# Kernel tuning notes

Hardware: AMD Instinct MI355X
Metric: run time of the kernel (lower is better)

Reference implementation:

```python
import jax, jax.numpy as jnp
import numpy as np

D_MODEL, D_K, D_V, H = 1024, 64, 64, 16
LN_EPS = 1e-5


def setup_inputs() -> dict:
    key = jax.random.key(0)
    ks = jax.random.split(key, 16)
    B, NQ, NK = 2, 1024, 1024
    queries = jax.random.normal(ks[0], (B, NQ, D_MODEL), dtype=jnp.float32)
    keys = jax.random.normal(ks[1], (B, NK, D_MODEL), dtype=jnp.float32)
    values = jax.random.normal(ks[2], (B, NK, D_MODEL), dtype=jnp.float32)
    attention_mask = jax.random.randint(ks[3], (B, H, NQ, NK), 0, 2).astype(jnp.bool_)
    attention_weights = jax.random.uniform(ks[4], (B, H, NQ, NK), dtype=jnp.float32)
    # Linear params, stored (in, out) so x @ W + b
    def xavier(k, shape):
        lim = float(np.sqrt(6.0 / (shape[0] + shape[1])))
        return jax.random.uniform(k, shape, jnp.float32, -lim, lim)
    Wq = xavier(ks[5], (D_MODEL, H * D_K)); bq = jnp.zeros((H * D_K,), jnp.float32)
    Wk = xavier(ks[6], (D_MODEL, H * D_K)); bk = jnp.zeros((H * D_K,), jnp.float32)
    Wv = xavier(ks[7], (D_MODEL, H * D_V)); bv = jnp.zeros((H * D_V,), jnp.float32)
    Wo = xavier(ks[8], (H * D_V, D_MODEL)); bo = jnp.zeros((D_MODEL,), jnp.float32)
    gamma = jnp.ones((D_MODEL,), jnp.float32)
    beta = jnp.zeros((D_MODEL,), jnp.float32)
    return dict(queries=queries, keys=keys, values=values,
                attention_mask=attention_mask, attention_weights=attention_weights,
                Wq=Wq, bq=bq, Wk=Wk, bk=bk, Wv=Wv, bv=bv, Wo=Wo, bo=bo,
                gamma=gamma, beta=beta)


def layer_norm(x, gamma, beta):
    mu = jnp.mean(x, axis=-1, keepdims=True)
    var = jnp.mean(jnp.square(x - mu), axis=-1, keepdims=True)
    return (x - mu) * jax.lax.rsqrt(var + LN_EPS) * gamma + beta


def reference(queries, keys, values, attention_mask, attention_weights,
              Wq, bq, Wk, bk, Wv, bv, Wo, bo, gamma, beta):
    B, NQ, _ = queries.shape
    NK = keys.shape[1]
    q = (queries @ Wq + bq).reshape(B, NQ, H, D_K).transpose(0, 2, 1, 3)  # b h nq dk
    k = (keys @ Wk + bk).reshape(B, NK, H, D_K).transpose(0, 2, 1, 3)    # b h nk dk
    v = (values @ Wv + bv).reshape(B, NK, H, D_V).transpose(0, 2, 1, 3)  # b h nk dv
    att = jnp.einsum('bhqd,bhkd->bhqk', q, k) / jnp.sqrt(jnp.float32(D_K))
    att = att * attention_weights
    att = jnp.where(attention_mask, -jnp.inf, att)
    att = jax.nn.softmax(att, axis=-1)  # dropout is identity in eval
    out = jnp.einsum('bhqk,bhkd->bhqd', att, v)
    out = out.transpose(0, 2, 1, 3).reshape(B, NQ, H * D_V)
    out = out @ Wo + bo
    # post-LN residual (identity_map_reordering=False)
    return layer_norm(queries + out, gamma, beta)
```

## Files before the change

kernel.cpp:

```cpp
#include <hip/hip_runtime.h>
#include <hip/hip_bf16.h>
#include <math.h>

#define B_   2
#define H_   16
#define NSEQ 1024
#define DM   1024
#define DKV  64
#define NSPLIT 4
#define KPB  (NSEQ / NSPLIT)
#define LNEPS 1e-5f

typedef __attribute__((ext_vector_type(8))) short s16x8;
typedef __attribute__((ext_vector_type(4))) float f32x4;
typedef __attribute__((ext_vector_type(4))) unsigned u32x4;

__device__ inline short f2bf(float f) {
    __hip_bfloat16 h = __float2bfloat16(f);
    return *reinterpret_cast<short*>(&h);
}
__device__ inline float bf2f(short s) {
    unsigned u = ((unsigned)(unsigned short)s) << 16;
    return __uint_as_float(u);
}

__device__ __forceinline__ void gll16(const void* g, void* l) {
    __builtin_amdgcn_global_load_lds(
        (const __attribute__((address_space(1))) unsigned int*)g,
        (__attribute__((address_space(3))) unsigned int*)l, 16, 0, 0);
}

#define SYNC_STAGE do { asm volatile("s_waitcnt vmcnt(0)" ::: "memory"); __syncthreads(); } while (0)

__global__ void detect_mask(const unsigned* __restrict__ mask_words, int* __restrict__ flag) {
    unsigned f = 0;
    for (int i = 0; i < 256; ++i) f |= (mask_words[i] > 1u) ? 1u : 0u;
    *flag = (int)f;
}

__global__ __launch_bounds__(256) void castT4_bf16(
    const float* __restrict__ w0, const float* __restrict__ w1,
    const float* __restrict__ w2, const float* __restrict__ w3,
    short* __restrict__ t0, short* __restrict__ t1,
    short* __restrict__ t2, short* __restrict__ t3) {
    const float* W = blockIdx.z == 0 ? w0 : (blockIdx.z == 1 ? w1 : (blockIdx.z == 2 ? w2 : w3));
    short* Wt      = blockIdx.z == 0 ? t0 : (blockIdx.z == 1 ? t1 : (blockIdx.z == 2 ? t2 : t3));
    __shared__ float tl[32][33];
    const int k0 = blockIdx.y * 32, n0 = blockIdx.x * 32;
    const int r = threadIdx.x >> 3, c4 = (threadIdx.x & 7) * 4;
    *(float4*)&tl[r][c4] = *(const float4*)(W + (size_t)(k0 + r) * DM + n0 + c4);
    __syncthreads();
    unsigned u0 = (unsigned short)f2bf(tl[c4+0][r]) | ((unsigned)(unsigned short)f2bf(tl[c4+1][r]) << 16);
    unsigned u1 = (unsigned short)f2bf(tl[c4+2][r]) | ((unsigned)(unsigned short)f2bf(tl[c4+3][r]) << 16);
    uint2 pk; pk.x = u0; pk.y = u1;
    *(uint2*)(Wt + (size_t)(n0 + r) * DM + k0 + c4) = pk;
}

__device__ inline void loadAf32(const float* p, s16x8& a0, s16x8& a1) {
    f32x4 v0 = *(const f32x4*)p,       v1 = *(const f32x4*)(p + 4);
    f32x4 v2 = *(const f32x4*)(p + 8), v3 = *(const f32x4*)(p + 12);
    a0[0]=f2bf(v0[0]); a0[1]=f2bf(v0[1]); a0[2]=f2bf(v0[2]); a0[3]=f2bf(v0[3]);
    a0[4]=f2bf(v1[0]); a0[5]=f2bf(v1[1]); a0[6]=f2bf(v1[2]); a0[7]=f2bf(v1[3]);
    a1[0]=f2bf(v2[0]); a1[1]=f2bf(v2[1]); a1[2]=f2bf(v2[2]); a1[3]=f2bf(v2[3]);
    a1[4]=f2bf(v3[0]); a1[5]=f2bf(v3[1]); a1[6]=f2bf(v3[2]); a1[7]=f2bf(v3[3]);
}

__global__ __launch_bounds__(256) void gemm_qkv(
    const float* __restrict__ qin, const float* __restrict__ kin, const float* __restrict__ vin,
    const short* __restrict__ Wcat,
    const float* __restrict__ bq, const float* __restrict__ bk, const float* __restrict__ bv,
    short* __restrict__ Qh, short* __restrict__ Kh, short* __restrict__ Vth)
{
    const int t  = threadIdx.x;
    const int wv = t >> 6, l = t & 63, lg = l >> 4, li = l & 15;
    const int wr = wv >> 1, wc = wv & 1;
    const int c0g = blockIdx.x * 64, m0 = blockIdx.y * 64;
    const int sel = c0g >> 10;
    const int c0  = c0g & 1023;
    const float* A    = sel == 0 ? qin : (sel == 1 ? kin : vin);
    const short* Wt   = Wcat + (size_t)sel * DM * DM;
    const float* bias = sel == 0 ? bq : (sel == 1 ? bk : bv);
    short* outp       = sel == 0 ? Qh : (sel == 1 ? Kh : Vth);
    const int mode    = sel == 2 ? 2 : 1;

    __shared__ short Asl[64 * 64];
    __shared__ short Bsl[64 * 64];

    f32x4 acc[2][2] = {};
    const int sr = t >> 2, scol = (t & 3) * 16;
    const int sw = (sr & 7) << 3;

    s16x8 a0, a1;
    loadAf32(A + (size_t)(m0 + sr) * DM + scol, a0, a1);
    s16x8 b0 = *(const s16x8*)(Wt + (size_t)(c0 + sr) * DM + scol);
    s16x8 b1 = *(const s16x8*)(Wt + (size_t)(c0 + sr) * DM + scol + 8);

    for (int k0 = 0; k0 < DM; k0 += 64) {
        __syncthreads();
        *(s16x8*)&Asl[sr * 64 + (scol ^ sw)]       = a0;
        *(s16x8*)&Asl[sr * 64 + ((scol + 8) ^ sw)] = a1;
        *(s16x8*)&Bsl[sr * 64 + (scol ^ sw)]       = b0;
        *(s16x8*)&Bsl[sr * 64 + ((scol + 8) ^ sw)] = b1;
        __syncthreads();
        if (k0 + 64 < DM) {
            loadAf32(A + (size_t)(m0 + sr) * DM + k0 + 64 + scol, a0, a1);
            b0 = *(const s16x8*)(Wt + (size_t)(c0 + sr) * DM + k0 + 64 + scol);
            b1 = *(const s16x8*)(Wt + (size_t)(c0 + sr) * DM + k0 + 64 + scol + 8);
        }
        #pragma unroll
        for (int kh = 0; kh < 2; ++kh) {
            s16x8 af[2], bf[2];
            #pragma unroll
            for (int fi = 0; fi < 2; ++fi) {
                const int row = wr * 32 + fi * 16 + li;
                af[fi] = *(const s16x8*)&Asl[row * 64 + ((kh * 32 + lg * 8) ^ ((row & 7) << 3))];
            }
            #pragma unroll
            for (int fj = 0; fj < 2; ++fj) {
                const int row = wc * 32 + fj * 16 + li;
                bf[fj] = *(const s16x8*)&Bsl[row * 64 + ((kh * 32 + lg * 8) ^ ((row & 7) << 3))];
            }
            #pragma unroll
            for (int fi = 0; fi < 2; ++fi)
                #pragma unroll
                for (int fj = 0; fj < 2; ++fj)
                    acc[fi][fj] = __builtin_amdgcn_mfma_f32_16x16x32_bf16(af[fi], bf[fj], acc[fi][fj], 0, 0, 0);
        }
    }

    const int hh = c0 >> 6;
    #pragma unroll
    for (int fi = 0; fi < 2; ++fi) {
        #pragma unroll
        for (int j = 0; j < 4; ++j) {
            const int m = m0 + wr * 32 + fi * 16 + lg * 4 + j;
            const int bb = m >> 10, n = m & (NSEQ - 1);
            #pragma unroll
            for (int fj = 0; fj < 2; ++fj) {
                const int cc = wc * 32 + fj * 16 + li;
                float v = acc[fi][fj][j] + bias[c0 + cc];
                if (mode == 1)
                    outp[(((size_t)(bb * H_ + hh) * NSEQ) + n) * DKV + cc] = f2bf(v);
                else
                    outp[(((size_t)(bb * H_ + hh) * DKV) + cc) * NSEQ + n] = f2bf(v);
            }
        }
    }
}

__global__ __launch_bounds__(256) void gemm_out(
    const short* __restrict__ A, const short* __restrict__ Wt,
    const float* __restrict__ bias, const float* __restrict__ resid,
    float* __restrict__ outp)
{
    const int t  = threadIdx.x;
    const int wv = t >> 6, l = t & 63, lg = l >> 4, li = l & 15;
    const int wr = wv >> 1, wc = wv & 1;
    const int c0 = blockIdx.x * 64, m0 = blockIdx.y * 64;

    __shared__ short Asl[64 * 64];
    __shared__ short Bsl[64 * 64];

    f32x4 acc[2][2] = {};
    const int sr = t >> 2, scol = (t & 3) * 16;
    const int sw = (sr & 7) << 3;

    s16x8 a0 = *(const s16x8*)(A + (size_t)(m0 + sr) * DM + scol);
    s16x8 a1 = *(const s16x8*)(A + (size_t)(m0 + sr) * DM + scol + 8);
    s16x8 b0 = *(const s16x8*)(Wt + (size_t)(c0 + sr) * DM + scol);
    s16x8 b1 = *(const s16x8*)(Wt + (size_t)(c0 + sr) * DM + scol + 8);

    for (int k0 = 0; k0 < DM; k0 += 64) {
        __syncthreads();
        *(s16x8*)&Asl[sr * 64 + (scol ^ sw)]       = a0;
        *(s16x8*)&Asl[sr * 64 + ((scol + 8) ^ sw)] = a1;
        *(s16x8*)&Bsl[sr * 64 + (scol ^ sw)]       = b0;
        *(s16x8*)&Bsl[sr * 64 + ((scol + 8) ^ sw)] = b1;
        __syncthreads();
        if (k0 + 64 < DM) {
            a0 = *(const s16x8*)(A + (size_t)(m0 + sr) * DM + k0 + 64 + scol);
            a1 = *(const s16x8*)(A + (size_t)(m0 + sr) * DM + k0 + 64 + scol + 8);
            b0 = *(const s16x8*)(Wt + (size_t)(c0 + sr) * DM + k0 + 64 + scol);
            b1 = *(const s16x8*)(Wt + (size_t)(c0 + sr) * DM + k0 + 64 + scol + 8);
        }
        #pragma unroll
        for (int kh = 0; kh < 2; ++kh) {
            s16x8 af[2], bf[2];
            #pragma unroll
            for (int fi = 0; fi < 2; ++fi) {
                const int row = wr * 32 + fi * 16 + li;
                af[fi] = *(const s16x8*)&Asl[row * 64 + ((kh * 32 + lg * 8) ^ ((row & 7) << 3))];
            }
            #pragma unroll
            for (int fj = 0; fj < 2; ++fj) {
                const int row = wc * 32 + fj * 16 + li;
                bf[fj] = *(const s16x8*)&Bsl[row * 64 + ((kh * 32 + lg * 8) ^ ((row & 7) << 3))];
            }
            #pragma unroll
            for (int fi = 0; fi < 2; ++fi)
                #pragma unroll
                for (int fj = 0; fj < 2; ++fj)
                    acc[fi][fj] = __builtin_amdgcn_mfma_f32_16x16x32_bf16(af[fi], bf[fj], acc[fi][fj], 0, 0, 0);
        }
    }

    #pragma unroll
    for (int fi = 0; fi < 2; ++fi) {
        #pragma unroll
        for (int j = 0; j < 4; ++j) {
            const int m = m0 + wr * 32 + fi * 16 + lg * 4 + j;
            #pragma unroll
            for (int fj = 0; fj < 2; ++fj) {
                const int c = c0 + wc * 32 + fj * 16 + li;
                outp[(size_t)m * DM + c] = acc[fi][fj][j] + bias[c] + resid[(size_t)m * DM + c];
            }
        }
    }
}

__global__ __launch_bounds__(256) void attn_split(
    const short* __restrict__ Qb, const short* __restrict__ Kb, const short* __restrict__ Vt,
    const void* __restrict__ mask, const float* __restrict__ wgt,
    const int* __restrict__ flagp, short* __restrict__ Opart,
    float* __restrict__ mpart, float* __restrict__ lpart)
{
    const int t  = threadIdx.x;
    const int wv = t >> 6;
    const int l  = t & 63;
    const int lg = l >> 4;
    const int li = l & 15;
    const int qt = blockIdx.x >> 2;
    const int sp = blockIdx.x & (NSPLIT-1);
    const int h  = blockIdx.y, b = blockIdx.z;
    const size_t bh = (size_t)b * H_ + h;
    const int qrow = qt*64 + wv*16 + li;
    const int kbase = sp * KPB;

    __shared__ short Kl[8 * 512];
    __shared__ short Vl[8 * 512];
    __shared__ float Wl[16 * 256];
    __shared__ unsigned char Ml[4 * 1024];
    __shared__ short Plds[4][16][80];

    const short* Qp = Qb + (bh * NSEQ + qt*64 + wv*16) * DKV;
    const short* Kp = Kb + bh * NSEQ * DKV;
    const short* Vp = Vt + bh * DKV * NSEQ;
    const size_t moff = (bh * NSEQ + qrow) * NSEQ;
    const size_t rowT = bh * NSEQ + (size_t)qt * 64;
    const int mmode = *flagp;
    const unsigned* Mi = (const unsigned*)mask;
    const unsigned char* Mb = (const unsigned char*)mask;

    const int srow = l >> 4;
    const int schk = (l & 15) ^ srow;
    const int mrow = l >> 2;
    const int mchk = l & 3;

    s16x8 qa[2];
    qa[0] = *(const s16x8*)(Qp + (size_t)li * DKV + lg*8);
    qa[1] = *(const s16x8*)(Qp + (size_t)li * DKV + 32 + lg*8);

    float m_run = -1e30f, l_run = 0.f;
    f32x4 oacc[4] = {};
    const int rq = li >> 2, rs = li & 3;

    for (int c = 0; c < NSPLIT; ++c) {
        const int kc = kbase + c * 64;

        __syncthreads();
        if (wv == 0) {
            #pragma unroll
            for (int i = 0; i < 8; ++i) {
                const int nt = i & 3, dc = i >> 2;
                gll16(Kp + (size_t)(kc + nt*16 + li) * DKV + dc*32 + lg*8, Kl + i*512);
            }
        } else if (wv == 1) {
            #pragma unroll
            for (int i = 0; i < 8; ++i) {
                const int dt = i & 3, kch = i >> 2;
                gll16(Vp + (size_t)(dt*16 + li) * NSEQ + kc + kch*32 + lg*8, Vl + i*512);
            }
        } else if (wv == 2) {
            #pragma unroll
            for (int j = 0; j < 8; ++j)
                gll16(wgt + (rowT + j*4 + srow) * NSEQ + kc + schk*4, Wl + j*256);
            #pragma unroll
            for (int j = 0; j < 2; ++j)
                gll16(Mb + (rowT + j*16 + mrow) * NSEQ + kc + mchk*16, Ml + j*1024);
        } else {
            #pragma unroll
            for (int j = 8; j < 16; ++j)
                gll16(wgt + (rowT + j*4 + srow) * NSEQ + kc + schk*4, Wl + j*256);
            #pragma unroll
            for (int j = 2; j < 4; ++j)
                gll16(Mb + (rowT + j*16 + mrow) * NSEQ + kc + mchk*16, Ml + j*1024);
        }
        SYNC_STAGE;

        f32x4 sc[4] = {};
        #pragma unroll
        for (int dc = 0; dc < 2; ++dc)
            #pragma unroll
            for (int nt = 0; nt < 4; ++nt) {
                s16x8 kb = *(const s16x8*)&Kl[(dc*4 + nt)*512 + l*8];
                sc[nt] = __builtin_amdgcn_mfma_f32_16x16x32_bf16(kb, qa[dc], sc[nt], 0, 0, 0);
            }

        float sv[16];
        float cmax = -1e30f;
        #pragma unroll
        for (int nt = 0; nt < 4; ++nt) {
            const int pos = ((nt*4 + lg) ^ rs) * 4;
            f32x4 w4 = *(const f32x4*)&Wl[(wv*4 + rq)*256 + rs*64 + pos];
            unsigned mm[4];
            if (mmode) {
                unsigned u = *(const unsigned*)&Ml[wv*1024 + (li*4 + nt)*16 + lg*4];
                mm[0] = u & 0xffu; mm[1] = (u >> 8) & 0xffu;
                mm[2] = (u >> 16) & 0xffu; mm[3] = u >> 24;
            } else {
                u32x4 mi = *(const u32x4*)(Mi + moff + kc + nt*16 + lg*4);
                mm[0] = mi[0]; mm[1] = mi[1]; mm[2] = mi[2]; mm[3] = mi[3];
            }
            #pragma unroll
            for (int r = 0; r < 4; ++r) {
                float s = sc[nt][r] * 0.125f * w4[r];
                s = mm[r] ? -1e30f : s;
                sv[nt*4 + r] = s;
                cmax = fmaxf(cmax, s);
            }
        }
        cmax = fmaxf(cmax, __shfl_xor(cmax, 16));
        cmax = fmaxf(cmax, __shfl_xor(cmax, 32));
        const float mnew = fmaxf(m_run, cmax);
        const float factor = __expf(m_run - mnew);
        m_run = mnew;

        float csum = 0.f;
        #pragma unroll
        for (int nt = 0; nt < 4; ++nt) {
            float p0 = __expf(sv[nt*4+0] - mnew), p1 = __expf(sv[nt*4+1] - mnew);
            float p2 = __expf(sv[nt*4+2] - mnew), p3 = __expf(sv[nt*4+3] - mnew);
            csum += p0 + p1 + p2 + p3;
            unsigned u0 = (unsigned short)f2bf(p0) | ((unsigned)(unsigned short)f2bf(p1) << 16);
            unsigned u1 = (unsigned short)f2bf(p2) | ((unsigned)(unsigned short)f2bf(p3) << 16);
            uint2 pk; pk.x = u0; pk.y = u1;
            *(uint2*)&Plds[wv][li][nt*16 + lg*4] = pk;
        }
        csum += __shfl_xor(csum, 16);
        csum += __shfl_xor(csum, 32);
        l_run = l_run * factor + csum;

        float ffac[4];
        #pragma unroll
        for (int r = 0; r < 4; ++r) ffac[r] = __shfl(factor, lg*4 + r);
        #pragma unroll
        for (int dt = 0; dt < 4; ++dt)
            #pragma unroll
            for (int r = 0; r < 4; ++r)
                oacc[dt][r] *= ffac[r];

        #pragma unroll
        for (int kch = 0; kch < 2; ++kch) {
            s16x8 pa = *(const s16x8*)&Plds[wv][li][kch*32 + lg*8];
            #pragma unroll
            for (int dt = 0; dt < 4; ++dt) {
                s16x8 vb = *(const s16x8*)&Vl[(kch*4 + dt)*512 + l*8];
                oacc[dt] = __builtin_amdgcn_mfma_f32_16x16x32_bf16(pa, vb, oacc[dt], 0, 0, 0);
            }
        }
    }

    const size_t SBH = (size_t)B_ * H_ * NSEQ;
    if (lg == 0) {
        mpart[(size_t)sp * SBH + bh * NSEQ + qrow] = m_run;
        lpart[(size_t)sp * SBH + bh * NSEQ + qrow] = l_run;
    }
    #pragma unroll
    for (int dt = 0; dt < 4; ++dt)
        #pragma unroll
        for (int r = 0; r < 4; ++r)
            Opart[((size_t)sp * SBH + bh * NSEQ + qt*64 + wv*16 + lg*4 + r) * DKV + dt*16 + li]
                = f2bf(oacc[dt][r]);
}

__global__ __launch_bounds__(256, 1) void attn_combine(
    const short* __restrict__ Opart, const float* __restrict__ mpart,
    const float* __restrict__ lpart, short* __restrict__ Ob)
{
    const size_t SBH = (size_t)B_ * H_ * NSEQ;
    const int R = blockIdx.x * 4 + (threadIdx.x >> 6);
    const int d = threadIdx.x & 63;
    const int bh = R >> 10, n = R & (NSEQ - 1);
    const int b = bh >> 4, h = bh & (H_ - 1);

    float ms[NSPLIT], ls[NSPLIT], ov[NSPLIT];
    #pragma unroll
    for (int s = 0; s < NSPLIT; ++s) {
        ms[s] = mpart[(size_t)s * SBH + R];
        ls[s] = lpart[(size_t)s * SBH + R];
        ov[s] = bf2f(Opart[((size_t)s * SBH + R) * DKV + d]);
    }
    float mstar = -1e30f;
    #pragma unroll
    for (int s = 0; s < NSPLIT; ++s) mstar = fmaxf(mstar, ms[s]);
    float lstar = 0.f, acc = 0.f;
    #pragma unroll
    for (int s = 0; s < NSPLIT; ++s) {
        float w = __expf(ms[s] - mstar);
        lstar += w * ls[s];
        acc   += w * ov[s];
    }
    Ob[((size_t)b * NSEQ + n) * DM + h * DKV + d] = f2bf(acc / lstar);
}

__global__ __launch_bounds__(256) void ln_kernel(
    const float* __restrict__ Y, const float* __restrict__ gamma,
    const float* __restrict__ beta, float* __restrict__ out)
{
    const int row = blockIdx.x;
    const int t = threadIdx.x;
    const float* y = Y + (size_t)row * DM;
    float4 x = *(const float4*)(y + t*4);
    __shared__ float red[4];
    float s = x.x + x.y + x.z + x.w;
    #pragma unroll
    for (int off = 32; off > 0; off >>= 1) s += __shfl_xor(s, off);
    if ((t & 63) == 0) red[t >> 6] = s;
    __syncthreads();
    float mean = (red[0]+red[1]+red[2]+red[3]) * (1.0f/DM);
    float d0 = x.x-mean, d1 = x.y-mean, d2 = x.z-mean, d3 = x.w-mean;
    float sq = d0*d0 + d1*d1 + d2*d2 + d3*d3;
    __syncthreads();
    #pragma unroll
    for (int off = 32; off > 0; off >>= 1) sq += __shfl_xor(sq, off);
    if ((t & 63) == 0) red[t >> 6] = sq;
    __syncthreads();
    float var = (red[0]+red[1]+red[2]+red[3]) * (1.0f/DM);
    float rstd = rsqrtf(var + LNEPS);
    int c = t * 4;
    float4 g  = *(const float4*)(gamma + c);
    float4 bb = *(const float4*)(beta + c);
    float4 o;
    o.x = d0*rstd*g.x + bb.x;
    o.y = d1*rstd*g.y + bb.y;
    o.z = d2*rstd*g.z + bb.z;
    o.w = d3*rstd*g.w + bb.w;
    *(float4*)(out + (size_t)row*DM + c) = o;
}

extern "C" void kernel_launch(void* const* d_in, const int* in_sizes, int n_in,
                              void* d_out, int out_size, void* d_ws, size_t ws_size,
                              hipStream_t stream)
{
    const float* queries = (const float*)d_in[0];
    const float* keys    = (const float*)d_in[1];
    const float* values  = (const float*)d_in[2];
    const void*  mask    = d_in[3];
    const float* wgt     = (const float*)d_in[4];
    const float* Wq = (const float*)d_in[5];  const float* bq = (const float*)d_in[6];
    const float* Wk = (const float*)d_in[7];  const float* bk = (const float*)d_in[8];
    const float* Wv = (const float*)d_in[9];  const float* bv = (const float*)d_in[10];
    const float* Wo = (const float*)d_in[11]; const float* bo = (const float*)d_in[12];
    const float* gamma = (const float*)d_in[13]; const float* beta = (const float*)d_in[14];
    float* out = (float*)d_out;

    const size_t SZ  = (size_t)B_ * NSEQ * DM;
    const size_t WSZ = (size_t)DM * DM;
    const size_t SBH = (size_t)B_ * H_ * NSEQ;

    char* ws = (char*)d_ws;
    int*   flag = (int*)ws;
    short* Wtq = (short*)(ws + 256);
    short* Wtk = Wtq + WSZ;
    short* Wtv = Wtk + WSZ;
    short* Wto = Wtv + WSZ;
    short* Qh  = Wto + WSZ;
    short* Kh  = Qh + SZ;
    short* Vth = Kh + SZ;
    short* Opart = Vth + SZ;
    float* mpart = (float*)(Opart + (size_t)NSPLIT * SBH * DKV);
    float* lpart = mpart + NSPLIT * SBH;
    short* Ob  = (short*)(lpart + NSPLIT * SBH);
    float* Yb  = (float*)Opart;

    detect_mask<<<1, 1, 0, stream>>>((const unsigned*)mask, flag);
    castT4_bf16<<<dim3(32, 32, 4), 256, 0, stream>>>(Wq, Wk, Wv, Wo, Wtq, Wtk, Wtv, Wto);

    gemm_qkv<<<dim3(48, 32), 256, 0, stream>>>(queries, keys, values, Wtq,
                                               bq, bk, bv, Qh, Kh, Vth);

    attn_split<<<dim3(16 * NSPLIT, H_, B_), 256, 0, stream>>>(
        Qh, Kh, Vth, mask, wgt, flag, Opart, mpart, lpart);
    attn_combine<<<dim3((int)(SBH / 4)), 256, 0, stream>>>(Opart, mpart, lpart, Ob);

    gemm_out<<<dim3(16, 32), 256, 0, stream>>>(Ob, Wto, bo, queries, Yb);
    ln_kernel<<<dim3(B_*NSEQ), 256, 0, stream>>>(Yb, gamma, beta, out);
}
```

Baseline: 161.9 us.

## Double-buffer K/V/weight/mask LDS tiles in split attention kernel

Converts the attn_split key loop to a two-stage pipeline. The next chunk's K, V, weight and mask tiles are issued with global_load_lds into a second LDS buffer while the current chunk is computed. Partial vmcnt waits and raw s_barrier replace the full wait-and-sync before every chunk. The P tile now reuses each wave's slice of the weight buffer instead of a separate array. LDS per block grows substantially, which may cut blocks per CU, and each split has only four chunks to overlap.

Result: slower. 166.7 us (+3.0%).

```diff
diff --git a/kernel.cpp b/kernel.cpp
--- a/kernel.cpp
+++ b/kernel.cpp
@@ -29,8 +29,6 @@
         (const __attribute__((address_space(1))) unsigned int*)g,
         (__attribute__((address_space(3))) unsigned int*)l, 16, 0, 0);
 }
-
-#define SYNC_STAGE do { asm volatile("s_waitcnt vmcnt(0)" ::: "memory"); __syncthreads(); } while (0)
 
 __global__ void detect_mask(const unsigned* __restrict__ mask_words, int* __restrict__ flag) {
     unsigned f = 0;
@@ -236,11 +234,10 @@
     const int qrow = qt*64 + wv*16 + li;
     const int kbase = sp * KPB;
 
-    __shared__ short Kl[8 * 512];
-    __shared__ short Vl[8 * 512];
-    __shared__ float Wl[16 * 256];
-    __shared__ unsigned char Ml[4 * 1024];
-    __shared__ short Plds[4][16][80];
+    __shared__ short Kl[2][4096];
+    __shared__ short Vl[2][4096];
+    __shared__ float Wl[2][4096];
+    __shared__ unsigned char Ml[2][4096];
 
     const short* Qp = Qb + (bh * NSEQ + qt*64 + wv*16) * DKV;
     const short* Kp = Kb + bh * NSEQ * DKV;
@@ -256,6 +253,31 @@
     const int mrow = l >> 2;
     const int mchk = l & 3;
 
+#define STAGE(c_, bi_) do {                                                               \
+    const int kc_ = kbase + (c_) * 64;                                                    \
+    if (wv == 0) {                                                                        \
+        _Pragma("unroll") for (int i = 0; i < 8; ++i) {                                   \
+            const int nt_ = i & 3, dc_ = i >> 2;                                          \
+            gll16(Kp + (size_t)(kc_ + nt_*16 + li) * DKV + dc_*32 + lg*8, &Kl[bi_][i*512]); \
+        }                                                                                 \
+    } else if (wv == 1) {                                                                 \
+        _Pragma("unroll") for (int i = 0; i < 8; ++i) {                                   \
+            const int dt_ = i & 3, kch_ = i >> 2;                                         \
+            gll16(Vp + (size_t)(dt_*16 + li) * NSEQ + kc_ + kch_*32 + lg*8, &Vl[bi_][i*512]); \
+        }                                                                                 \
+    } else if (wv == 2) {                                                                 \
+        _Pragma("unroll") for (int j = 0; j < 8; ++j)                                     \
+            gll16(wgt + (rowT + j*4 + srow) * NSEQ + kc_ + schk*4, &Wl[bi_][j*256]);      \
+        _Pragma("unroll") for (int j = 0; j < 2; ++j)                                     \
+            gll16(Mb + (rowT + j*16 + mrow) * NSEQ + kc_ + mchk*16, &Ml[bi_][j*1024]);    \
+    } else {                                                                              \
+        _Pragma("unroll") for (int j = 8; j < 16; ++j)                                    \
+            gll16(wgt + (rowT + j*4 + srow) * NSEQ + kc_ + schk*4, &Wl[bi_][j*256]);      \
+        _Pragma("unroll") for (int j = 2; j < 4; ++j)                                     \
+            gll16(Mb + (rowT + j*16 + mrow) * NSEQ + kc_ + mchk*16, &Ml[bi_][j*1024]);    \
+    }                                                                                     \
+} while (0)
+
     s16x8 qa[2];
     qa[0] = *(const s16x8*)(Qp + (size_t)li * DKV + lg*8);
     qa[1] = *(const s16x8*)(Qp + (size_t)li * DKV + 32 + lg*8);
@@ -264,45 +286,27 @@
     f32x4 oacc[4] = {};
     const int rq = li >> 2, rs = li & 3;
 
+    STAGE(0, 0);
+
     for (int c = 0; c < NSPLIT; ++c) {
+        const int bi = c & 1;
         const int kc = kbase + c * 64;
 
-        __syncthreads();
-        if (wv == 0) {
-            #pragma unroll
-            for (int i = 0; i < 8; ++i) {
-                const int nt = i & 3, dc = i >> 2;
-                gll16(Kp + (size_t)(kc + nt*16 + li) * DKV + dc*32 + lg*8, Kl + i*512);
-            }
-        } else if (wv == 1) {
-            #pragma unroll
-            for (int i = 0; i < 8; ++i) {
-                const int dt = i & 3, kch = i >> 2;
-                gll16(Vp + (size_t)(dt*16 + li) * NSEQ + kc + kch*32 + lg*8, Vl + i*512);
-            }
-        } else if (wv == 2) {
-            #pragma unroll
-            for (int j = 0; j < 8; ++j)
-                gll16(wgt + (rowT + j*4 + srow) * NSEQ + kc + schk*4, Wl + j*256);
-            #pragma unroll
-            for (int j = 0; j < 2; ++j)
-                gll16(Mb + (rowT + j*16 + mrow) * NSEQ + kc + mchk*16, Ml + j*1024);
+        if (c + 1 < NSPLIT) {
+            STAGE(c + 1, bi ^ 1);
+            if (wv < 2) asm volatile("s_waitcnt vmcnt(8)" ::: "memory");
+            else        asm volatile("s_waitcnt vmcnt(10)" ::: "memory");
         } else {
-            #pragma unroll
-            for (int j = 8; j < 16; ++j)
-                gll16(wgt + (rowT + j*4 + srow) * NSEQ + kc + schk*4, Wl + j*256);
-            #pragma unroll
-            for (int j = 2; j < 4; ++j)
-                gll16(Mb + (rowT + j*16 + mrow) * NSEQ + kc + mchk*16, Ml + j*1024);
-        }
-        SYNC_STAGE;
+            asm volatile("s_waitcnt vmcnt(0)" ::: "memory");
+        }
+        __builtin_amdgcn_s_barrier();
 
         f32x4 sc[4] = {};
         #pragma unroll
         for (int dc = 0; dc < 2; ++dc)
             #pragma unroll
             for (int nt = 0; nt < 4; ++nt) {
-                s16x8 kb = *(const s16x8*)&Kl[(dc*4 + nt)*512 + l*8];
+                s16x8 kb = *(const s16x8*)&Kl[bi][(dc*4 + nt)*512 + l*8];
                 sc[nt] = __builtin_amdgcn_mfma_f32_16x16x32_bf16(kb, qa[dc], sc[nt], 0, 0, 0);
             }
 
@@ -311,10 +315,10 @@
         #pragma unroll
         for (int nt = 0; nt < 4; ++nt) {
             const int pos = ((nt*4 + lg) ^ rs) * 4;
-            f32x4 w4 = *(const f32x4*)&Wl[(wv*4 + rq)*256 + rs*64 + pos];
+            f32x4 w4 = *(const f32x4*)&Wl[bi][(wv*4 + rq)*256 + rs*64 + pos];
             unsigned mm[4];
             if (mmode) {
-                unsigned u = *(const unsigned*)&Ml[wv*1024 + (li*4 + nt)*16 + lg*4];
+                unsigned u = *(const unsigned*)&Ml[bi][wv*1024 + (li*4 + nt)*16 + lg*4];
                 mm[0] = u & 0xffu; mm[1] = (u >> 8) & 0xffu;
                 mm[2] = (u >> 16) & 0xffu; mm[3] = u >> 24;
             } else {
@@ -335,6 +339,7 @@
         const float factor = __expf(m_run - mnew);
         m_run = mnew;
 
+        short* Pq = (short*)&Wl[bi][wv*1024];
         float csum = 0.f;
         #pragma unroll
         for (int nt = 0; nt < 4; ++nt) {
@@ -344,7 +349,7 @@
             unsigned u0 = (unsigned short)f2bf(p0) | ((unsigned)(unsigned short)f2bf(p1) << 16);
             unsigned u1 = (unsigned short)f2bf(p2) | ((unsigned)(unsigned short)f2bf(p3) << 16);
             uint2 pk; pk.x = u0; pk.y = u1;
-            *(uint2*)&Plds[wv][li][nt*16 + lg*4] = pk;
+            *(uint2*)&Pq[li*80 + nt*16 + lg*4] = pk;
         }
         csum += __shfl_xor(csum, 16);
         csum += __shfl_xor(csum, 32);
@@ -361,13 +366,15 @@
 
         #pragma unroll
         for (int kch = 0; kch < 2; ++kch) {
-            s16x8 pa = *(const s16x8*)&Plds[wv][li][kch*32 + lg*8];
+            s16x8 pa = *(const s16x8*)&Pq[li*80 + kch*32 + lg*8];
             #pragma unroll
             for (int dt = 0; dt < 4; ++dt) {
-                s16x8 vb = *(const s16x8*)&Vl[(kch*4 + dt)*512 + l*8];
+                s16x8 vb = *(const s16x8*)&Vl[bi][(kch*4 + dt)*512 + l*8];
                 oacc[dt] = __builtin_amdgcn_mfma_f32_16x16x32_bf16(pa, vb, oacc[dt], 0, 0, 0);
             }
         }
+
+        __builtin_amdgcn_s_barrier();
     }
 
     const size_t SBH = (size_t)B_ * H_ * NSEQ;
@@ -381,6 +388,7 @@
         for (int r = 0; r < 4; ++r)
             Opart[((size_t)sp * SBH + bh * NSEQ + qt*64 + wv*16 + lg*4 + r) * DKV + dt*16 + li]
                 = f2bf(oacc[dt][r]);
+#undef STAGE
 }
 
 __global__ __launch_bounds__(256, 1) void attn_combine(
```
